# Kernel optimization log

Measured on AMD Instinct MI355X. Metric: run time of the kernel, lower is better.

## Reference

```python
import jax, jax.numpy as jnp
import numpy as np
from jax import lax

FEAT = 384        # features
FFN = 768         # ffn_features (chunk=True -> halves of 384)
ZDIM = FFN // 2   # 384
HID = 192         # AE hidden
B, N = 4, 128
LN_EPS = 1e-5


def gelu(x):
    return jax.nn.gelu(x, approximate=False)  # torch nn.GELU default = exact erf


def setup_inputs() -> dict:
    key = jax.random.key(0)
    ks = jax.random.split(key, 12)

    def lin(k, fan_in, shape):
        bound = 1.0 / np.sqrt(fan_in)
        return jax.random.uniform(k, shape, jnp.float32, -bound, bound)

    return {
        "x": jax.random.normal(ks[0], (B, N, FEAT), jnp.float32),
        "U_w": lin(ks[1], FEAT, (FEAT, FFN)),
        "U_b": lin(ks[2], FEAT, (FFN,)),
        "ln_w": jnp.ones((ZDIM,), jnp.float32),
        "ln_b": jnp.zeros((ZDIM,), jnp.float32),
        "enc_w": lin(ks[3], ZDIM, (ZDIM, HID)),
        "enc_b": lin(ks[4], ZDIM, (HID,)),
        "dec_w": lin(ks[5], HID, (HID, ZDIM)),
        "dec_b": lin(ks[6], HID, (ZDIM,)),
        "V_w": lin(ks[7], ZDIM, (ZDIM, FEAT)),
        "V_b": lin(ks[8], ZDIM, (FEAT,)),
    }


def _ae(z, enc_w, enc_b, dec_w, dec_b):
    h = gelu(z @ enc_w + enc_b)
    return h @ dec_w + dec_b


def reference(x, U_w, U_b, ln_w, ln_b, enc_w, enc_b, dec_w, dec_b, V_w, V_b):
    h = gelu(x @ U_w + U_b)                    # (B,N,FFN)
    xh, z = jnp.split(h, 2, axis=-1)           # chunk=True: (B,N,ZDIM) each
    z = lax.stop_gradient(z)                   # z.detach()
    mu = jnp.mean(z, axis=-1, keepdims=True)
    var = jnp.var(z, axis=-1, keepdims=True)
    z = (z - mu) / jnp.sqrt(var + LN_EPS) * ln_w + ln_b

    n = z.shape[1]
    eye = jnp.eye(n, dtype=z.dtype)
    # z_mask[b,i,j,:] = z[b,j,:] if i==j else 0   (mask_type='zeros')
    z_mask = eye[None, :, :, None] * z[:, None, :, :]   # (B,N,N,ZDIM)
    preds = _ae(z_mask, enc_w, enc_b, dec_w, dec_b)      # (B,N,N,ZDIM)
    dist = jnp.einsum('bijf,bjf->bij', preds, z)         # (B,N,N)
    attn = lax.stop_gradient(jax.nn.softmax(dist, axis=-1))
    out = jnp.einsum('bij,bjf->bif', attn, xh)           # (B,N,ZDIM)
    return out @ V_w + V_b                               # (B,N,FEAT)
```

## Files before the change

kernel.cpp:

```cpp
#include <hip/hip_runtime.h>
#include <hip/hip_bf16.h>
#include <math.h>

#define FEAT 384
#define FFN  768
#define ZDIM 384
#define HID  192
#define BB   4
#define NN   128
#define BN   (BB*NN)

__device__ __forceinline__ float gelu_exact(float x) {
    return 0.5f * x * (1.0f + erff(x * 0.70710678118654752440f));
}

__device__ __forceinline__ float bflo(unsigned u) { return __uint_as_float(u << 16); }
__device__ __forceinline__ float bfhi(unsigned u) { return __uint_as_float(u & 0xFFFF0000u); }

template<bool F32>
__device__ __forceinline__ float ldg(const void* p, int i) {
    if constexpr (F32) return ((const float*)p)[i];
    return __uint_as_float(((unsigned)((const unsigned short*)p)[i]) << 16);
}
template<bool F32>
__device__ __forceinline__ void stg(void* p, size_t i, float v) {
    if constexpr (F32) ((float*)p)[i] = v;
    else ((__hip_bfloat16*)p)[i] = __float2bfloat16(v);
}

template<bool F32> struct V4;
template<> struct V4<true> {
    float4 a;
    __device__ __forceinline__ void load(const void* p, size_t off) {
        a = *(const float4*)((const float*)p + off);
    }
    __device__ __forceinline__ float g(int i) const { return (&a.x)[i]; }
};
template<> struct V4<false> {
    uint2 u;
    __device__ __forceinline__ void load(const void* p, size_t off) {
        u = *(const uint2*)((const unsigned short*)p + off);
    }
    __device__ __forceinline__ float g(int i) const {
        const unsigned w = (&u.x)[i >> 1];
        return (i & 1) ? bfhi(w) : bflo(w);
    }
};

__device__ __forceinline__ bool is_f32(const void* ln_w) {
    return ((const unsigned short*)ln_w)[0] == 0;
}

__device__ __forceinline__ float block_sum(float v, float* sm) {
    for (int o = 32; o > 0; o >>= 1) v += __shfl_down(v, o, 64);
    const int lane = threadIdx.x & 63, w = threadIdx.x >> 6;
    __syncthreads();
    if (lane == 0) sm[w] = v;
    __syncthreads();
    return sm[0] + sm[1] + sm[2] + sm[3] + sm[4] + sm[5];
}
__device__ __forceinline__ float block_max(float v, float* sm) {
    for (int o = 32; o > 0; o >>= 1) v = fmaxf(v, __shfl_down(v, o, 64));
    const int lane = threadIdx.x & 63, w = threadIdx.x >> 6;
    __syncthreads();
    if (lane == 0) sm[w] = v;
    __syncthreads();
    return fmaxf(fmaxf(fmaxf(sm[0], sm[1]), fmaxf(sm[2], sm[3])), fmaxf(sm[4], sm[5]));
}
__device__ __forceinline__ void block_sum8(const float v[8], float* sm, float out[8]) {
    float tv[8];
    #pragma unroll
    for (int n = 0; n < 8; n++) tv[n] = v[n];
    for (int o = 32; o > 0; o >>= 1) {
        #pragma unroll
        for (int n = 0; n < 8; n++) tv[n] += __shfl_down(tv[n], o, 64);
    }
    const int lane = threadIdx.x & 63, w = threadIdx.x >> 6;
    __syncthreads();
    if (lane == 0) {
        #pragma unroll
        for (int n = 0; n < 8; n++) sm[n * 6 + w] = tv[n];
    }
    __syncthreads();
    #pragma unroll
    for (int n = 0; n < 8; n++)
        out[n] = sm[n*6] + sm[n*6+1] + sm[n*6+2] + sm[n*6+3] + sm[n*6+4] + sm[n*6+5];
}

#define SM_TOTAL 9840

template<bool F32, int KCH, int M>
__device__ __forceinline__ void gemmMx4(
    const void* __restrict__ W, int ldw, int c0, int kb,
    const float* __restrict__ in, int ldin, float acc[M][4])
{
    constexpr int NB = KCH / 8;
    V4<F32> buf[3][8];
    #pragma unroll
    for (int j = 0; j < 8; j++) buf[0][j].load(W, (size_t)(kb + j) * ldw + c0);
    if (NB > 1) {
        #pragma unroll
        for (int j = 0; j < 8; j++) buf[1][j].load(W, (size_t)(kb + 8 + j) * ldw + c0);
    }
    #pragma unroll
    for (int b = 0; b < NB; b++) {
        const int cur = b % 3;
        if (b + 2 < NB) {
            const int nxt = (b + 2) % 3;
            #pragma unroll
            for (int j = 0; j < 8; j++)
                buf[nxt][j].load(W, (size_t)(kb + (b + 2) * 8 + j) * ldw + c0);
        }
        #pragma unroll
        for (int m = 0; m < M; m++) {
            const float4 x0 = *(const float4*)(in + m * ldin + kb + b * 8);
            const float4 x1 = *(const float4*)(in + m * ldin + kb + b * 8 + 4);
            const float xv[8] = {x0.x, x0.y, x0.z, x0.w, x1.x, x1.y, x1.z, x1.w};
            #pragma unroll
            for (int j = 0; j < 8; j++) {
                #pragma unroll
                for (int i = 0; i < 4; i++)
                    acc[m][i] = fmaf(xv[j], buf[cur][j].g(i), acc[m][i]);
            }
        }
    }
}

template<bool F32>
__device__ void bodyA(float* S, int q,
    const void* __restrict__ x, const void* __restrict__ U_w,
    const void* __restrict__ U_b, const void* __restrict__ ln_w,
    const void* __restrict__ ln_b, const void* __restrict__ enc_w,
    const void* __restrict__ enc_b, const void* __restrict__ dec_w,
    const void* __restrict__ dec_b,
    float* __restrict__ d0, float* __restrict__ diag)
{
    const int rb = 4 * q;
    const int t = threadIdx.x;
    float* xs = S;
    float* zs = S + 1536;
    float* hid = S + 3072;
    float* gh = S + 3840;
    float* part = S + 4032;
    float* sm = S + 9792;

    #pragma unroll
    for (int m = 0; m < 4; m++) xs[m * 384 + t] = ldg<F32>(x, (rb + m) * FEAT + t);
    if (t < HID) gh[t] = gelu_exact(ldg<F32>(enc_b, t));
    __syncthreads();

    const int cg = t % 96, kh = t / 96;
    const int cL = 4 * cg, cG = ZDIM + cL, kb = 96 * kh;
    float acc[4][4] = {};
    gemmMx4<F32, 96, 4>(U_w, FFN, cG, kb, xs, 384, acc);
    if (kh > 0) {
        float* p = &part[(kh - 1) * 1536 + cg];
        #pragma unroll
        for (int m = 0; m < 4; m++)
            #pragma unroll
            for (int i = 0; i < 4; i++) p[(m * 4 + i) * 96] = acc[m][i];
    }
    __syncthreads();

    float hv[4][4];
    float sv[8] = {};
    if (kh == 0) {
        #pragma unroll
        for (int i = 0; i < 4; i++) {
            const float ub = ldg<F32>(U_b, cG + i);
            #pragma unroll
            for (int m = 0; m < 4; m++) {
                float v = acc[m][i] + ub
                        + part[(m * 4 + i) * 96 + cg]
                        + part[1536 + (m * 4 + i) * 96 + cg]
                        + part[3072 + (m * 4 + i) * 96 + cg];
                v = gelu_exact(v);
                hv[m][i] = v;
                sv[m] += v;
                sv[4 + m] += v * v;
            }
        }
    }
    float SS[8];
    block_sum8(sv, sm, SS);
    if (kh == 0) {
        #pragma unroll
        for (int m = 0; m < 4; m++) {
            const float mu = SS[m] * (1.0f / ZDIM);
            const float rs = rsqrtf(SS[4 + m] * (1.0f / ZDIM) - mu * mu + 1e-5f);
            #pragma unroll
            for (int i = 0; i < 4; i++) {
                const int zc = cL + i;
                zs[m * 384 + zc] = (hv[m][i] - mu) * rs * ldg<F32>(ln_w, zc) + ldg<F32>(ln_b, zc);
            }
        }
    }
    __syncthreads();

    {
        const int cgE = t % 48, khE = t / 48;
        const int cE = 4 * cgE, kbE = 48 * khE;
        float ea[4][4] = {};
        gemmMx4<F32, 48, 4>(enc_w, HID, cE, kbE, zs, 384, ea);
        if (khE > 0) {
            float* p = &part[(khE - 1) * 768 + cgE];
            #pragma unroll
            for (int m = 0; m < 4; m++)
                #pragma unroll
                for (int i = 0; i < 4; i++) p[(m * 4 + i) * 48] = ea[m][i];
        }
        __syncthreads();
        if (khE == 0) {
            #pragma unroll
            for (int i = 0; i < 4; i++) {
                const float ebv = ldg<F32>(enc_b, cE + i);
                #pragma unroll
                for (int m = 0; m < 4; m++) {
                    float v = ea[m][i] + ebv;
                    #pragma unroll
                    for (int kk = 0; kk < 7; kk++)
                        v += part[kk * 768 + (m * 4 + i) * 48 + cgE];
                    hid[m * 192 + cE + i] = gelu_exact(v);
                }
            }
        }
        __syncthreads();
    }

    {
        const int cgD = t % 96, khD = t / 96;
        const int cD = 4 * cgD, kbD = 48 * khD;
        float da[5][4] = {};
        gemmMx4<F32, 48, 5>(dec_w, ZDIM, cD, kbD, hid, 192, da);
        if (khD > 0) {
            float* p = &part[(khD - 1) * 1920 + cgD];
            #pragma unroll
            for (int m = 0; m < 5; m++)
                #pragma unroll
                for (int i = 0; i < 4; i++) p[(m * 4 + i) * 96] = da[m][i];
        }
        __syncthreads();
        float dv[8] = {};
        if (khD == 0) {
            #pragma unroll
            for (int i = 0; i < 4; i++) {
                const int c = cD + i;
                const float dbv = ldg<F32>(dec_b, c);
                float vc = da[4][i] + dbv;
                #pragma unroll
                for (int kk = 0; kk < 3; kk++)
                    vc += part[kk * 1920 + (16 + i) * 96 + cgD];
                #pragma unroll
                for (int m = 0; m < 4; m++) {
                    float v = da[m][i] + dbv;
                    #pragma unroll
                    for (int kk = 0; kk < 3; kk++)
                        v += part[kk * 1920 + (m * 4 + i) * 96 + cgD];
                    const float zv = zs[m * 384 + c];
                    dv[m] = fmaf(v, zv, dv[m]);
                    dv[4 + m] = fmaf(vc, zv, dv[4 + m]);
                }
            }
        }
        float DD8[8];
        block_sum8(dv, sm, DD8);
        if (t == 0) {
            #pragma unroll
            for (int m = 0; m < 4; m++) { diag[rb + m] = DD8[m]; d0[rb + m] = DD8[4 + m]; }
        }
    }
}

template<bool F32>
__device__ void bodyB(float* S, int q,
    const void* __restrict__ x, const void* __restrict__ U_w,
    const void* __restrict__ U_b, const void* __restrict__ V_w,
    float* __restrict__ Y)
{
    const int rb = 4 * q;
    const int t = threadIdx.x;
    float* xs = S;
    float* zs = S + 1536;
    float* part = S + 4032;

    #pragma unroll
    for (int m = 0; m < 4; m++) xs[m * 384 + t] = ldg<F32>(x, (rb + m) * FEAT + t);
    __syncthreads();

    const int cg = t % 96, kh = t / 96;
    const int cL = 4 * cg, kb = 96 * kh;
    float acc[4][4] = {};
    gemmMx4<F32, 96, 4>(U_w, FFN, cL, kb, xs, 384, acc);
    if (kh > 0) {
        float* p = &part[(kh - 1) * 1536 + cg];
        #pragma unroll
        for (int m = 0; m < 4; m++)
            #pragma unroll
            for (int i = 0; i < 4; i++) p[(m * 4 + i) * 96] = acc[m][i];
    }
    __syncthreads();
    if (kh == 0) {
        #pragma unroll
        for (int i = 0; i < 4; i++) {
            const float ub = ldg<F32>(U_b, cL + i);
            #pragma unroll
            for (int m = 0; m < 4; m++) {
                float v = acc[m][i] + ub
                        + part[(m * 4 + i) * 96 + cg]
                        + part[1536 + (m * 4 + i) * 96 + cg]
                        + part[3072 + (m * 4 + i) * 96 + cg];
                zs[m * 384 + cL + i] = gelu_exact(v);
            }
        }
    }
    __syncthreads();

    float ya[4][4] = {};
    gemmMx4<F32, 96, 4>(V_w, FEAT, cL, kb, zs, 384, ya);
    if (kh > 0) {
        float* p = &part[(kh - 1) * 1536 + cg];
        #pragma unroll
        for (int m = 0; m < 4; m++)
            #pragma unroll
            for (int i = 0; i < 4; i++) p[(m * 4 + i) * 96] = ya[m][i];
    }
    __syncthreads();
    if (kh == 0) {
        #pragma unroll
        for (int m = 0; m < 4; m++) {
            float o[4];
            #pragma unroll
            for (int i = 0; i < 4; i++) {
                o[i] = ya[m][i]
                     + part[(m * 4 + i) * 96 + cg]
                     + part[1536 + (m * 4 + i) * 96 + cg]
                     + part[3072 + (m * 4 + i) * 96 + cg];
            }
            *(float4*)(Y + (size_t)(rb + m) * FEAT + cL) = make_float4(o[0], o[1], o[2], o[3]);
        }
    }
}

__global__ __launch_bounds__(384) void k_main(
    const void* x, const void* U_w, const void* U_b,
    const void* ln_w, const void* ln_b,
    const void* enc_w, const void* enc_b,
    const void* dec_w, const void* dec_b, const void* V_w,
    float* Y, float* d0, float* diag)
{
    __shared__ float S[SM_TOTAL];
    const int type = blockIdx.x & 1;
    const int q = blockIdx.x >> 1;
    if (is_f32(ln_w)) {
        if (type == 0) bodyA<true >(S, q, x, U_w, U_b, ln_w, ln_b, enc_w, enc_b, dec_w, dec_b, d0, diag);
        else           bodyB<true >(S, q, x, U_w, U_b, V_w, Y);
    } else {
        if (type == 0) bodyA<false>(S, q, x, U_w, U_b, ln_w, ln_b, enc_w, enc_b, dec_w, dec_b, d0, diag);
        else           bodyB<false>(S, q, x, U_w, U_b, V_w, Y);
    }
}

template<bool F32>
__device__ void combine_body(
    const float* __restrict__ d0, const float* __restrict__ diag,
    const float* __restrict__ Y,
    const void* __restrict__ V_b, void* __restrict__ out)
{
    const int b  = blockIdx.x >> 4;
    const int cc = (blockIdx.x & 15) * 24;
    const int t = threadIdx.x;
    const int c = t % 24, qq = t / 24;
    __shared__ float e0s[NN], eds[NN];
    __shared__ float bp[16 * 24];
    __shared__ float baseY[24];
    __shared__ float sm[12];

    float d0v = -INFINITY, dgv = -INFINITY;
    if (t < NN) { d0v = d0[b * NN + t]; dgv = diag[b * NN + t]; }
    const float m = block_max(fmaxf(d0v, dgv), sm);
    float e0v = 0.f;
    if (t < NN) {
        e0v = expf(d0v - m);
        e0s[t] = e0v;
        eds[t] = expf(dgv - m);
    }
    const float S = block_sum(e0v, sm);

    const float* Yb = Y + (size_t)b * NN * FEAT + cc + c;
    const int j0 = 8 * qq;
    float w[8];
    #pragma unroll
    for (int j = 0; j < 8; j++) w[j] = Yb[(size_t)(j0 + j) * FEAT];
    float p = 0.f;
    #pragma unroll
    for (int j = 0; j < 8; j++) p = fmaf(e0s[j0 + j], w[j], p);
    bp[qq * 24 + c] = p;
    __syncthreads();
    if (qq == 0) {
        float s = 0.f;
        #pragma unroll
        for (int g = 0; g < 16; g++) s += bp[g * 24 + c];
        baseY[c] = s;
    }
    __syncthreads();

    const float bY = baseY[c];
    const float vb = ldg<F32>(V_b, cc + c);
    #pragma unroll
    for (int j = 0; j < 8; j++) {
        const int r = j0 + j;
        const float inv = 1.0f / (S - e0s[r] + eds[r]);
        const float val = (bY + (eds[r] - e0s[r]) * w[j]) * inv + vb;
        stg<F32>(out, (size_t)(b * NN + r) * FEAT + cc + c, val);
    }
}

__global__ __launch_bounds__(384) void k_combine(
    const void* ln_w,
    const float* d0, const float* diag, const float* Y,
    const void* V_b, void* out)
{
    if (is_f32(ln_w))
        combine_body<true >(d0, diag, Y, V_b, out);
    else
        combine_body<false>(d0, diag, Y, V_b, out);
}

extern "C" void kernel_launch(void* const* d_in, const int* in_sizes, int n_in,
                              void* d_out, int out_size, void* d_ws, size_t ws_size,
                              hipStream_t stream) {
    const void* x     = d_in[0];
    const void* U_w   = d_in[1];
    const void* U_b   = d_in[2];
    const void* ln_w  = d_in[3];
    const void* ln_b  = d_in[4];
    const void* enc_w = d_in[5];
    const void* enc_b = d_in[6];
    const void* dec_w = d_in[7];
    const void* dec_b = d_in[8];
    const void* V_w   = d_in[9];
    const void* V_b   = d_in[10];

    float* ws   = (float*)d_ws;
    float* Y    = ws;
    float* d0   = Y + (size_t)BN * FEAT;
    float* diag = d0 + BN;

    k_main<<<2 * (BN / 4), 384, 0, stream>>>(x, U_w, U_b, ln_w, ln_b, enc_w, enc_b,
                                             dec_w, dec_b, V_w, Y, d0, diag);
    k_combine<<<16 * BB, 384, 0, stream>>>(ln_w, d0, diag, Y, V_b, d_out);
}
```

Baseline: 103.3 us.

## Split fused main kernel into two stages with 8-row tiles and algebraic AE dot

Replaces the single fused kernel (256 blocks of 4 rows each) with two kernels. Stage 1 computes U-projection tiles of 8 rows by 96 columns across 512 blocks and transposes enc_w/dec_w into a combined weight buffer. Stage 2 runs the LayerNorm plus autoencoder path and the V-projection as 8-row blocks split over hidden or column tiles, with the AE diagonal term written as gelu(enc)·(dec_w·z) partial sums reduced in the combine kernel. The aim is more parallelism and better weight reuse per block. The cost is an extra launch and global round-trips for xh, z0 and the weight transpose.

```diff
diff --git a/kernel.cpp b/kernel.cpp
--- a/kernel.cpp
+++ b/kernel.cpp
@@ -10,6 +10,7 @@
 #define NN   128
 #define BN   (BB*NN)
 
+
 __device__ __forceinline__ float gelu_exact(float x) {
     return 0.5f * x * (1.0f + erff(x * 0.70710678118654752440f));
 }
@@ -18,7 +19,7 @@
 __device__ __forceinline__ float bfhi(unsigned u) { return __uint_as_float(u & 0xFFFF0000u); }
 
 template<bool F32>
-__device__ __forceinline__ float ldg(const void* p, int i) {
+__device__ __forceinline__ float ldg(const void* p, size_t i) {
     if constexpr (F32) return ((const float*)p)[i];
     return __uint_as_float(((unsigned)((const unsigned short*)p)[i]) << 16);
 }
@@ -47,6 +48,19 @@
     }
 };
 
+template<bool F32>
+__device__ __forceinline__ void load8(const void* p, size_t i, float o[8]) {
+    if constexpr (F32) {
+        const float4 a = *(const float4*)((const float*)p + i);
+        const float4 b = *(const float4*)((const float*)p + i + 4);
+        o[0]=a.x;o[1]=a.y;o[2]=a.z;o[3]=a.w;o[4]=b.x;o[5]=b.y;o[6]=b.z;o[7]=b.w;
+    } else {
+        const uint4 u = *(const uint4*)((const unsigned short*)p + i);
+        o[0]=bflo(u.x);o[1]=bfhi(u.x);o[2]=bflo(u.y);o[3]=bfhi(u.y);
+        o[4]=bflo(u.z);o[5]=bfhi(u.z);o[6]=bflo(u.w);o[7]=bfhi(u.w);
+    }
+}
+
 __device__ __forceinline__ bool is_f32(const void* ln_w) {
     return ((const unsigned short*)ln_w)[0] == 0;
 }
@@ -67,55 +81,52 @@
     __syncthreads();
     return fmaxf(fmaxf(fmaxf(sm[0], sm[1]), fmaxf(sm[2], sm[3])), fmaxf(sm[4], sm[5]));
 }
-__device__ __forceinline__ void block_sum8(const float v[8], float* sm, float out[8]) {
-    float tv[8];
-    #pragma unroll
-    for (int n = 0; n < 8; n++) tv[n] = v[n];
+__device__ __forceinline__ void block_sum16(const float v[16], float* sm, float out[16]) {
+    float tv[16];
+    #pragma unroll
+    for (int n = 0; n < 16; n++) tv[n] = v[n];
     for (int o = 32; o > 0; o >>= 1) {
         #pragma unroll
-        for (int n = 0; n < 8; n++) tv[n] += __shfl_down(tv[n], o, 64);
+        for (int n = 0; n < 16; n++) tv[n] += __shfl_down(tv[n], o, 64);
     }
     const int lane = threadIdx.x & 63, w = threadIdx.x >> 6;
     __syncthreads();
     if (lane == 0) {
         #pragma unroll
-        for (int n = 0; n < 8; n++) sm[n * 6 + w] = tv[n];
-    }
-    __syncthreads();
-    #pragma unroll
-    for (int n = 0; n < 8; n++)
+        for (int n = 0; n < 16; n++) sm[n * 6 + w] = tv[n];
+    }
+    __syncthreads();
+    #pragma unroll
+    for (int n = 0; n < 16; n++)
         out[n] = sm[n*6] + sm[n*6+1] + sm[n*6+2] + sm[n*6+3] + sm[n*6+4] + sm[n*6+5];
 }
 
-#define SM_TOTAL 9840
-
-template<bool F32, int KCH, int M>
-__device__ __forceinline__ void gemmMx4(
-    const void* __restrict__ W, int ldw, int c0, int kb,
-    const float* __restrict__ in, int ldin, float acc[M][4])
-{
-    constexpr int NB = KCH / 8;
-    V4<F32> buf[3][8];
-    #pragma unroll
-    for (int j = 0; j < 8; j++) buf[0][j].load(W, (size_t)(kb + j) * ldw + c0);
-    if (NB > 1) {
-        #pragma unroll
-        for (int j = 0; j < 8; j++) buf[1][j].load(W, (size_t)(kb + 8 + j) * ldw + c0);
-    }
-    #pragma unroll
-    for (int b = 0; b < NB; b++) {
-        const int cur = b % 3;
-        if (b + 2 < NB) {
-            const int nxt = (b + 2) % 3;
+template<bool F32>
+__device__ __forceinline__ void tile_gemm_8x96(
+    const void* __restrict__ W, int ldw, int c0,
+    const float* __restrict__ xs, float* __restrict__ part, float out2[2])
+{
+    const int t = threadIdx.x;
+    const int cg = t % 24, kh = t / 24;
+    const int kb = kh * 24;
+    const int cc = c0 + 4 * cg;
+    float acc[8][4] = {};
+    V4<F32> buf[2][8];
+    #pragma unroll
+    for (int j = 0; j < 8; j++) buf[0][j].load(W, (size_t)(kb + j) * ldw + cc);
+    #pragma unroll
+    for (int b = 0; b < 3; b++) {
+        const int cur = b & 1;
+        if (b < 2) {
             #pragma unroll
             for (int j = 0; j < 8; j++)
-                buf[nxt][j].load(W, (size_t)(kb + (b + 2) * 8 + j) * ldw + c0);
-        }
-        #pragma unroll
-        for (int m = 0; m < M; m++) {
-            const float4 x0 = *(const float4*)(in + m * ldin + kb + b * 8);
-            const float4 x1 = *(const float4*)(in + m * ldin + kb + b * 8 + 4);
-            const float xv[8] = {x0.x, x0.y, x0.z, x0.w, x1.x, x1.y, x1.z, x1.w};
+                buf[cur ^ 1][j].load(W, (size_t)(kb + 8 * (b + 1) + j) * ldw + cc);
+        }
+        #pragma unroll
+        for (int m = 0; m < 8; m++) {
+            const float4 x0 = *(const float4*)(xs + m * 384 + kb + 8 * b);
+            const float4 x1 = *(const float4*)(xs + m * 384 + kb + 8 * b + 4);
+            const float xv[8] = {x0.x,x0.y,x0.z,x0.w,x1.x,x1.y,x1.z,x1.w};
             #pragma unroll
             for (int j = 0; j < 8; j++) {
                 #pragma unroll
@@ -124,245 +135,226 @@
             }
         }
     }
-}
-
-template<bool F32>
-__device__ void bodyA(float* S, int q,
-    const void* __restrict__ x, const void* __restrict__ U_w,
-    const void* __restrict__ U_b, const void* __restrict__ ln_w,
-    const void* __restrict__ ln_b, const void* __restrict__ enc_w,
-    const void* __restrict__ enc_b, const void* __restrict__ dec_w,
-    const void* __restrict__ dec_b,
-    float* __restrict__ d0, float* __restrict__ diag)
-{
-    const int rb = 4 * q;
+    #pragma unroll
+    for (int m = 0; m < 8; m++)
+        *(float4*)(part + kh * 768 + m * 96 + 4 * cg) =
+            make_float4(acc[m][0], acc[m][1], acc[m][2], acc[m][3]);
+    __syncthreads();
+    #pragma unroll
+    for (int s = 0; s < 2; s++) {
+        const int u = t + 384 * s;
+        float v = 0.f;
+        #pragma unroll
+        for (int k2 = 0; k2 < 16; k2++) v += part[k2 * 768 + u];
+        out2[s] = v;
+    }
+}
+
+#define S_LDS 15360
+
+template<bool F32>
+__device__ void stage1_body(const void* __restrict__ x, const void* __restrict__ U_w,
+                            const void* __restrict__ U_b,
+                            const void* __restrict__ enc_w, const void* __restrict__ dec_w,
+                            float* __restrict__ xh, float* __restrict__ z0,
+                            float* __restrict__ WEG, float* S)
+{
+    const int bid = blockIdx.x, t = threadIdx.x;
+    if (bid >= 512) {
+        if (bid < 560) {
+            const int h0 = (bid - 512) * 4;
+            V4<F32> w; w.load(enc_w, (size_t)t * HID + h0);
+            #pragma unroll
+            for (int j = 0; j < 4; j++) WEG[(size_t)(h0 + j) * 384 + t] = w.g(j);
+        } else {
+            const int r0 = (bid - 560) * 4;
+            #pragma unroll
+            for (int j = 0; j < 4; j++)
+                WEG[(size_t)(192 + r0 + j) * 384 + t] =
+                    ldg<F32>(dec_w, (size_t)(r0 + j) * ZDIM + t);
+        }
+        return;
+    }
+    float* xs = S;
+    float* part = S + 3072;
+    const int rowg = bid >> 3, colt = bid & 7;
+    const int rb = rowg * 8;
+    {
+        const int r = t / 48, c8 = 8 * (t % 48);
+        float xv[8]; load8<F32>(x, (size_t)(rb + r) * FEAT + c8, xv);
+        #pragma unroll
+        for (int j = 0; j < 8; j++) xs[r * 384 + c8 + j] = xv[j];
+    }
+    __syncthreads();
+    float out2[2];
+    tile_gemm_8x96<F32>(U_w, FFN, colt * 96, xs, part, out2);
+    const int uhalf = (colt >= 4);
+    float* dst = uhalf ? z0 : xh;
+    const int cbase = colt * 96 - (uhalf ? 384 : 0);
+    #pragma unroll
+    for (int s = 0; s < 2; s++) {
+        const int u = t + 384 * s;
+        const int m = u / 96, col = u % 96;
+        const float v = out2[s] + ldg<F32>(U_b, colt * 96 + col);
+        dst[(size_t)(rb + m) * 384 + cbase + col] = gelu_exact(v);
+    }
+}
+
+template<bool F32>
+__device__ void stage2z_body(const void* __restrict__ ln_w, const void* __restrict__ ln_b,
+                             const void* __restrict__ enc_b, const void* __restrict__ dec_b,
+                             const float* __restrict__ z0, const float* __restrict__ WEG,
+                             float* __restrict__ d0p, float* __restrict__ dgp,
+                             float* S, int q)
+{
+    const int rowg = q >> 2, ht = q & 3;
+    const int rb = rowg * 8, h0 = ht * 48;
+    const int t = threadIdx.x;
+    float* zs  = S;
+    float* pEG = S + 3072;
+    float* Es  = S + 6144;
+    float* Gs  = S + 6528;
+    float* sm  = S + 6912;
+
+    const int r = t / 48, c8 = 8 * (t % 48);
+    float zv[8];
+    {
+        const float4 a = *(const float4*)(z0 + (size_t)(rb + r) * 384 + c8);
+        const float4 b = *(const float4*)(z0 + (size_t)(rb + r) * 384 + c8 + 4);
+        zv[0]=a.x;zv[1]=a.y;zv[2]=a.z;zv[3]=a.w;zv[4]=b.x;zv[5]=b.y;zv[6]=b.z;zv[7]=b.w;
+    }
+    float s1 = 0.f, s2 = 0.f;
+    #pragma unroll
+    for (int j = 0; j < 8; j++) { s1 += zv[j]; s2 += zv[j] * zv[j]; }
+    float sv[16] = {}; sv[r] = s1; sv[8 + r] = s2;
+    float SS[16];
+    block_sum16(sv, sm, SS);
+    const float mu = SS[r] * (1.0f / ZDIM);
+    const float rs = rsqrtf(SS[8 + r] * (1.0f / ZDIM) - mu * mu + 1e-5f);
+    float lw[8], lb[8];
+    load8<F32>(ln_w, c8, lw);
+    load8<F32>(ln_b, c8, lb);
+    #pragma unroll
+    for (int j = 0; j < 8; j++)
+        zs[r * 384 + c8 + j] = (zv[j] - mu) * rs * lw[j] + lb[j];
+    __syncthreads();
+
+    const int hg = t % 96, kh = t / 96;
+    const int wrow = h0 + hg + (hg < 48 ? 0 : 144);
+    const float* Wr = WEG + (size_t)wrow * 384 + kh * 96;
+    float acc[8] = {};
+    float4 wb[2][4];
+    #pragma unroll
+    for (int j = 0; j < 4; j++) wb[0][j] = *(const float4*)(Wr + 4 * j);
+    #pragma unroll
+    for (int g = 0; g < 6; g++) {
+        const int cur = g & 1;
+        if (g < 5) {
+            #pragma unroll
+            for (int j = 0; j < 4; j++)
+                wb[cur ^ 1][j] = *(const float4*)(Wr + 16 * (g + 1) + 4 * j);
+        }
+        #pragma unroll
+        for (int j = 0; j < 4; j++) {
+            const int k = kh * 96 + 16 * g + 4 * j;
+            const float4 wq = wb[cur][j];
+            #pragma unroll
+            for (int rr = 0; rr < 8; rr++) {
+                const float4 zq = *(const float4*)(zs + rr * 384 + k);
+                acc[rr] = fmaf(zq.x, wq.x, fmaf(zq.y, wq.y,
+                          fmaf(zq.z, wq.z, fmaf(zq.w, wq.w, acc[rr]))));
+            }
+        }
+    }
+    #pragma unroll
+    for (int rr = 0; rr < 8; rr++) pEG[kh * 768 + rr * 96 + hg] = acc[rr];
+    __syncthreads();
+    #pragma unroll
+    for (int s = 0; s < 2; s++) {
+        const int u = t + 384 * s;
+        const int ur = u / 96, uh = u % 96;
+        const float v = pEG[u] + pEG[768 + u] + pEG[1536 + u] + pEG[2304 + u];
+        if (uh < 48) Es[ur * 48 + uh] = v + ldg<F32>(enc_b, h0 + uh);
+        else         Gs[ur * 48 + uh - 48] = v;
+    }
+    __syncthreads();
+    const int pr = t / 48, ph = t % 48;
+    const float gv = Gs[pr * 48 + ph];
+    float pd = gelu_exact(Es[pr * 48 + ph]) * gv;
+    float p0 = gelu_exact(ldg<F32>(enc_b, h0 + ph)) * gv;
+    if (ht == 0) {
+        float dbz = 0.f;
+        #pragma unroll
+        for (int j = 0; j < 8; j++) {
+            const int c = ph + 48 * j;
+            dbz = fmaf(ldg<F32>(dec_b, c), zs[pr * 384 + c], dbz);
+        }
+        pd += dbz; p0 += dbz;
+    }
+    float sv2[16] = {}; sv2[pr] = pd; sv2[8 + pr] = p0;
+    float SS2[16];
+    block_sum16(sv2, sm, SS2);
+    if (t < 8)            dgp[ht * BN + rb + t] = SS2[t];
+    else if (t < 16)      d0p[ht * BN + rb + (t - 8)] = SS2[8 + (t - 8)];
+}
+
+template<bool F32>
+__device__ void stage2y_body(const void* __restrict__ V_w, const float* __restrict__ xh,
+                             float* __restrict__ Y, float* S, int q)
+{
+    const int rowg = q >> 2, colt = q & 3;
+    const int rb = rowg * 8, c0 = colt * 96;
     const int t = threadIdx.x;
     float* xs = S;
-    float* zs = S + 1536;
-    float* hid = S + 3072;
-    float* gh = S + 3840;
-    float* part = S + 4032;
-    float* sm = S + 9792;
-
-    #pragma unroll
-    for (int m = 0; m < 4; m++) xs[m * 384 + t] = ldg<F32>(x, (rb + m) * FEAT + t);
-    if (t < HID) gh[t] = gelu_exact(ldg<F32>(enc_b, t));
-    __syncthreads();
-
-    const int cg = t % 96, kh = t / 96;
-    const int cL = 4 * cg, cG = ZDIM + cL, kb = 96 * kh;
-    float acc[4][4] = {};
-    gemmMx4<F32, 96, 4>(U_w, FFN, cG, kb, xs, 384, acc);
-    if (kh > 0) {
-        float* p = &part[(kh - 1) * 1536 + cg];
-        #pragma unroll
-        for (int m = 0; m < 4; m++)
-            #pragma unroll
-            for (int i = 0; i < 4; i++) p[(m * 4 + i) * 96] = acc[m][i];
-    }
-    __syncthreads();
-
-    float hv[4][4];
-    float sv[8] = {};
-    if (kh == 0) {
-        #pragma unroll
-        for (int i = 0; i < 4; i++) {
-            const float ub = ldg<F32>(U_b, cG + i);
-            #pragma unroll
-            for (int m = 0; m < 4; m++) {
-                float v = acc[m][i] + ub
-                        + part[(m * 4 + i) * 96 + cg]
-                        + part[1536 + (m * 4 + i) * 96 + cg]
-                        + part[3072 + (m * 4 + i) * 96 + cg];
-                v = gelu_exact(v);
-                hv[m][i] = v;
-                sv[m] += v;
-                sv[4 + m] += v * v;
-            }
-        }
-    }
-    float SS[8];
-    block_sum8(sv, sm, SS);
-    if (kh == 0) {
-        #pragma unroll
-        for (int m = 0; m < 4; m++) {
-            const float mu = SS[m] * (1.0f / ZDIM);
-            const float rs = rsqrtf(SS[4 + m] * (1.0f / ZDIM) - mu * mu + 1e-5f);
-            #pragma unroll
-            for (int i = 0; i < 4; i++) {
-                const int zc = cL + i;
-                zs[m * 384 + zc] = (hv[m][i] - mu) * rs * ldg<F32>(ln_w, zc) + ldg<F32>(ln_b, zc);
-            }
-        }
-    }
-    __syncthreads();
-
+    float* part = S + 3072;
     {
-        const int cgE = t % 48, khE = t / 48;
-        const int cE = 4 * cgE, kbE = 48 * khE;
-        float ea[4][4] = {};
-        gemmMx4<F32, 48, 4>(enc_w, HID, cE, kbE, zs, 384, ea);
-        if (khE > 0) {
-            float* p = &part[(khE - 1) * 768 + cgE];
-            #pragma unroll
-            for (int m = 0; m < 4; m++)
-                #pragma unroll
-                for (int i = 0; i < 4; i++) p[(m * 4 + i) * 48] = ea[m][i];
-        }
-        __syncthreads();
-        if (khE == 0) {
-            #pragma unroll
-            for (int i = 0; i < 4; i++) {
-                const float ebv = ldg<F32>(enc_b, cE + i);
-                #pragma unroll
-                for (int m = 0; m < 4; m++) {
-                    float v = ea[m][i] + ebv;
-                    #pragma unroll
-                    for (int kk = 0; kk < 7; kk++)
-                        v += part[kk * 768 + (m * 4 + i) * 48 + cgE];
-                    hid[m * 192 + cE + i] = gelu_exact(v);
-                }
-            }
-        }
-        __syncthreads();
-    }
-
-    {
-        const int cgD = t % 96, khD = t / 96;
-        const int cD = 4 * cgD, kbD = 48 * khD;
-        float da[5][4] = {};
-        gemmMx4<F32, 48, 5>(dec_w, ZDIM, cD, kbD, hid, 192, da);
-        if (khD > 0) {
-            float* p = &part[(khD - 1) * 1920 + cgD];
-            #pragma unroll
-            for (int m = 0; m < 5; m++)
-                #pragma unroll
-                for (int i = 0; i < 4; i++) p[(m * 4 + i) * 96] = da[m][i];
-        }
-        __syncthreads();
-        float dv[8] = {};
-        if (khD == 0) {
-            #pragma unroll
-            for (int i = 0; i < 4; i++) {
-                const int c = cD + i;
-                const float dbv = ldg<F32>(dec_b, c);
-                float vc = da[4][i] + dbv;
-                #pragma unroll
-                for (int kk = 0; kk < 3; kk++)
-                    vc += part[kk * 1920 + (16 + i) * 96 + cgD];
-                #pragma unroll
-                for (int m = 0; m < 4; m++) {
-                    float v = da[m][i] + dbv;
-                    #pragma unroll
-                    for (int kk = 0; kk < 3; kk++)
-                        v += part[kk * 1920 + (m * 4 + i) * 96 + cgD];
-                    const float zv = zs[m * 384 + c];
-                    dv[m] = fmaf(v, zv, dv[m]);
-                    dv[4 + m] = fmaf(vc, zv, dv[4 + m]);
-                }
-            }
-        }
-        float DD8[8];
-        block_sum8(dv, sm, DD8);
-        if (t == 0) {
-            #pragma unroll
-            for (int m = 0; m < 4; m++) { diag[rb + m] = DD8[m]; d0[rb + m] = DD8[4 + m]; }
-        }
-    }
-}
-
-template<bool F32>
-__device__ void bodyB(float* S, int q,
-    const void* __restrict__ x, const void* __restrict__ U_w,
-    const void* __restrict__ U_b, const void* __restrict__ V_w,
-    float* __restrict__ Y)
-{
-    const int rb = 4 * q;
-    const int t = threadIdx.x;
-    float* xs = S;
-    float* zs = S + 1536;
-    float* part = S + 4032;
-
-    #pragma unroll
-    for (int m = 0; m < 4; m++) xs[m * 384 + t] = ldg<F32>(x, (rb + m) * FEAT + t);
-    __syncthreads();
-
-    const int cg = t % 96, kh = t / 96;
-    const int cL = 4 * cg, kb = 96 * kh;
-    float acc[4][4] = {};
-    gemmMx4<F32, 96, 4>(U_w, FFN, cL, kb, xs, 384, acc);
-    if (kh > 0) {
-        float* p = &part[(kh - 1) * 1536 + cg];
-        #pragma unroll
-        for (int m = 0; m < 4; m++)
-            #pragma unroll
-            for (int i = 0; i < 4; i++) p[(m * 4 + i) * 96] = acc[m][i];
-    }
-    __syncthreads();
-    if (kh == 0) {
-        #pragma unroll
-        for (int i = 0; i < 4; i++) {
-            const float ub = ldg<F32>(U_b, cL + i);
-            #pragma unroll
-            for (int m = 0; m < 4; m++) {
-                float v = acc[m][i] + ub
-                        + part[(m * 4 + i) * 96 + cg]
-                        + part[1536 + (m * 4 + i) * 96 + cg]
-                        + part[3072 + (m * 4 + i) * 96 + cg];
-                zs[m * 384 + cL + i] = gelu_exact(v);
-            }
-        }
-    }
-    __syncthreads();
-
-    float ya[4][4] = {};
-    gemmMx4<F32, 96, 4>(V_w, FEAT, cL, kb, zs, 384, ya);
-    if (kh > 0) {
-        float* p = &part[(kh - 1) * 1536 + cg];
-        #pragma unroll
-        for (int m = 0; m < 4; m++)
-            #pragma unroll
-            for (int i = 0; i < 4; i++) p[(m * 4 + i) * 96] = ya[m][i];
-    }
-    __syncthreads();
-    if (kh == 0) {
-        #pragma unroll
-        for (int m = 0; m < 4; m++) {
-            float o[4];
-            #pragma unroll
-            for (int i = 0; i < 4; i++) {
-                o[i] = ya[m][i]
-                     + part[(m * 4 + i) * 96 + cg]
-                     + part[1536 + (m * 4 + i) * 96 + cg]
-                     + part[3072 + (m * 4 + i) * 96 + cg];
-            }
-            *(float4*)(Y + (size_t)(rb + m) * FEAT + cL) = make_float4(o[0], o[1], o[2], o[3]);
-        }
-    }
-}
-
-__global__ __launch_bounds__(384) void k_main(
-    const void* x, const void* U_w, const void* U_b,
-    const void* ln_w, const void* ln_b,
-    const void* enc_w, const void* enc_b,
-    const void* dec_w, const void* dec_b, const void* V_w,
-    float* Y, float* d0, float* diag)
-{
-    __shared__ float S[SM_TOTAL];
-    const int type = blockIdx.x & 1;
-    const int q = blockIdx.x >> 1;
+        const int r = t / 48, c8 = 8 * (t % 48);
+        const float4 a = *(const float4*)(xh + (size_t)(rb + r) * 384 + c8);
+        const float4 b = *(const float4*)(xh + (size_t)(rb + r) * 384 + c8 + 4);
+        *(float4*)(xs + r * 384 + c8) = a;
+        *(float4*)(xs + r * 384 + c8 + 4) = b;
+    }
+    __syncthreads();
+    float out2[2];
+    tile_gemm_8x96<F32>(V_w, FEAT, c0, xs, part, out2);
+    #pragma unroll
+    for (int s = 0; s < 2; s++) {
+        const int u = t + 384 * s;
+        const int m = u / 96, col = u % 96;
+        Y[(size_t)(rb + m) * 384 + c0 + col] = out2[s];
+    }
+}
+
+__global__ __launch_bounds__(384, 3) void k_stage1(
+    const void* x, const void* U_w, const void* U_b, const void* ln_w,
+    const void* enc_w, const void* dec_w,
+    float* xh, float* z0, float* WEG)
+{
+    __shared__ float S[S_LDS];
+    if (is_f32(ln_w)) stage1_body<true >(x, U_w, U_b, enc_w, dec_w, xh, z0, WEG, S);
+    else              stage1_body<false>(x, U_w, U_b, enc_w, dec_w, xh, z0, WEG, S);
+}
+
+__global__ __launch_bounds__(384, 3) void k_stage2(
+    const void* ln_w, const void* ln_b, const void* enc_b, const void* dec_b,
+    const void* V_w, const float* xh, const float* z0, const float* WEG,
+    float* Y, float* d0p, float* dgp)
+{
+    __shared__ float S[S_LDS];
+    const int type = blockIdx.x >> 8;
+    const int q = blockIdx.x & 255;
     if (is_f32(ln_w)) {
-        if (type == 0) bodyA<true >(S, q, x, U_w, U_b, ln_w, ln_b, enc_w, enc_b, dec_w, dec_b, d0, diag);
-        else           bodyB<true >(S, q, x, U_w, U_b, V_w, Y);
+        if (type == 0) stage2z_body<true >(ln_w, ln_b, enc_b, dec_b, z0, WEG, d0p, dgp, S, q);
+        else           stage2y_body<true >(V_w, xh, Y, S, q);
     } else {
-        if (type == 0) bodyA<false>(S, q, x, U_w, U_b, ln_w, ln_b, enc_w, enc_b, dec_w, dec_b, d0, diag);
-        else           bodyB<false>(S, q, x, U_w, U_b, V_w, Y);
+        if (type == 0) stage2z_body<false>(ln_w, ln_b, enc_b, dec_b, z0, WEG, d0p, dgp, S, q);
+        else           stage2y_body<false>(V_w, xh, Y, S, q);
     }
 }
 
 template<bool F32>
 __device__ void combine_body(
-    const float* __restrict__ d0, const float* __restrict__ diag,
+    const float* __restrict__ d0p, const float* __restrict__ dgp,
     const float* __restrict__ Y,
     const void* __restrict__ V_b, void* __restrict__ out)
 {
@@ -376,7 +368,15 @@
     __shared__ float sm[12];
 
     float d0v = -INFINITY, dgv = -INFINITY;
-    if (t < NN) { d0v = d0[b * NN + t]; dgv = diag[b * NN + t]; }
+    if (t < NN) {
+        float a0 = 0.f, ag = 0.f;
+        #pragma unroll
+        for (int ct = 0; ct < 4; ct++) {
+            a0 += d0p[ct * BN + b * NN + t];
+            ag += dgp[ct * BN + b * NN + t];
+        }
+        d0v = a0; dgv = ag;
+    }
     const float m = block_max(fmaxf(d0v, dgv), sm);
     float e0v = 0.f;
     if (t < NN) {
@@ -384,7 +384,7 @@
         e0s[t] = e0v;
         eds[t] = expf(dgv - m);
     }
-    const float S = block_sum(e0v, sm);
+    const float Ssum = block_sum(e0v, sm);
 
     const float* Yb = Y + (size_t)b * NN * FEAT + cc + c;
     const int j0 = 8 * qq;
@@ -409,7 +409,7 @@
     #pragma unroll
     for (int j = 0; j < 8; j++) {
         const int r = j0 + j;
-        const float inv = 1.0f / (S - e0s[r] + eds[r]);
+        const float inv = 1.0f / (Ssum - e0s[r] + eds[r]);
         const float val = (bY + (eds[r] - e0s[r]) * w[j]) * inv + vb;
         stg<F32>(out, (size_t)(b * NN + r) * FEAT + cc + c, val);
     }
@@ -417,13 +417,13 @@
 
 __global__ __launch_bounds__(384) void k_combine(
     const void* ln_w,
-    const float* d0, const float* diag, const float* Y,
+    const float* d0p, const float* dgp, const float* Y,
     const void* V_b, void* out)
 {
     if (is_f32(ln_w))
-        combine_body<true >(d0, diag, Y, V_b, out);
+        combine_body<true >(d0p, dgp, Y, V_b, out);
     else
-        combine_body<false>(d0, diag, Y, V_b, out);
+        combine_body<false>(d0p, dgp, Y, V_b, out);
 }
 
 extern "C" void kernel_launch(void* const* d_in, const int* in_sizes, int n_in,
@@ -441,12 +441,15 @@
     const void* V_w   = d_in[9];
     const void* V_b   = d_in[10];
 
-    float* ws   = (float*)d_ws;
-    float* Y    = ws;
-    float* d0   = Y + (size_t)BN * FEAT;
-    float* diag = d0 + BN;
-
-    k_main<<<2 * (BN / 4), 384, 0, stream>>>(x, U_w, U_b, ln_w, ln_b, enc_w, enc_b,
-                                             dec_w, dec_b, V_w, Y, d0, diag);
-    k_combine<<<16 * BB, 384, 0, stream>>>(ln_w, d0, diag, Y, V_b, d_out);
-}
+    float* ws  = (float*)d_ws;
+    float* xh  = ws;
+    float* z0  = xh  + 196608;
+    float* WEG = z0  + 196608;
+    float* Y   = WEG + 147456;
+    float* d0p = Y   + 196608;
+    float* dgp = d0p + 4 * BN;
+
+    k_stage1<<<608, 384, 0, stream>>>(x, U_w, U_b, ln_w, enc_w, dec_w, xh, z0, WEG);
+    k_stage2<<<512, 384, 0, stream>>>(ln_w, ln_b, enc_b, dec_b, V_w, xh, z0, WEG, Y, d0p, dgp);
+    k_combine<<<16 * BB, 384, 0, stream>>>(ln_w, d0p, dgp, Y, V_b, d_out);
+}
```

New measurement: 111.6 us. 1.08x slower.

## Fuse combine stage into main kernel via cooperative grid sync

Applied to the files above, without the earlier changes.

Merges the separate combine kernel into the main kernel. A cooperative launch and a grid-wide barrier replace the second kernel launch, and the first 64 blocks run the softmax/combine step after the barrier. This removes one launch and the gap between kernels. In exchange, all 256 blocks must be co-resident, and a grid sync on this hardware carries its own cost, which may match or exceed the launch gap it replaces.

```diff
diff --git a/kernel.cpp b/kernel.cpp
--- a/kernel.cpp
+++ b/kernel.cpp
@@ -1,5 +1,6 @@
 #include <hip/hip_runtime.h>
 #include <hip/hip_bf16.h>
+#include <hip/hip_cooperative_groups.h>
 #include <math.h>
 
 #define FEAT 384
@@ -341,27 +342,8 @@
     }
 }
 
-__global__ __launch_bounds__(384) void k_main(
-    const void* x, const void* U_w, const void* U_b,
-    const void* ln_w, const void* ln_b,
-    const void* enc_w, const void* enc_b,
-    const void* dec_w, const void* dec_b, const void* V_w,
-    float* Y, float* d0, float* diag)
-{
-    __shared__ float S[SM_TOTAL];
-    const int type = blockIdx.x & 1;
-    const int q = blockIdx.x >> 1;
-    if (is_f32(ln_w)) {
-        if (type == 0) bodyA<true >(S, q, x, U_w, U_b, ln_w, ln_b, enc_w, enc_b, dec_w, dec_b, d0, diag);
-        else           bodyB<true >(S, q, x, U_w, U_b, V_w, Y);
-    } else {
-        if (type == 0) bodyA<false>(S, q, x, U_w, U_b, ln_w, ln_b, enc_w, enc_b, dec_w, dec_b, d0, diag);
-        else           bodyB<false>(S, q, x, U_w, U_b, V_w, Y);
-    }
-}
-
 template<bool F32>
-__device__ void combine_body(
+__device__ void combine_body(float* S,
     const float* __restrict__ d0, const float* __restrict__ diag,
     const float* __restrict__ Y,
     const void* __restrict__ V_b, void* __restrict__ out)
@@ -370,10 +352,11 @@
     const int cc = (blockIdx.x & 15) * 24;
     const int t = threadIdx.x;
     const int c = t % 24, qq = t / 24;
-    __shared__ float e0s[NN], eds[NN];
-    __shared__ float bp[16 * 24];
-    __shared__ float baseY[24];
-    __shared__ float sm[12];
+    float* e0s   = S;
+    float* eds   = S + 128;
+    float* bp    = S + 256;
+    float* baseY = S + 640;
+    float* sm    = S + 664;
 
     float d0v = -INFINITY, dgv = -INFINITY;
     if (t < NN) { d0v = d0[b * NN + t]; dgv = diag[b * NN + t]; }
@@ -384,7 +367,7 @@
         e0s[t] = e0v;
         eds[t] = expf(dgv - m);
     }
-    const float S = block_sum(e0v, sm);
+    const float Ssum = block_sum(e0v, sm);
 
     const float* Yb = Y + (size_t)b * NN * FEAT + cc + c;
     const int j0 = 8 * qq;
@@ -409,21 +392,39 @@
     #pragma unroll
     for (int j = 0; j < 8; j++) {
         const int r = j0 + j;
-        const float inv = 1.0f / (S - e0s[r] + eds[r]);
+        const float inv = 1.0f / (Ssum - e0s[r] + eds[r]);
         const float val = (bY + (eds[r] - e0s[r]) * w[j]) * inv + vb;
         stg<F32>(out, (size_t)(b * NN + r) * FEAT + cc + c, val);
     }
 }
 
-__global__ __launch_bounds__(384) void k_combine(
-    const void* ln_w,
-    const float* d0, const float* diag, const float* Y,
-    const void* V_b, void* out)
+__global__ __launch_bounds__(384) void k_main(
+    const void* x, const void* U_w, const void* U_b,
+    const void* ln_w, const void* ln_b,
+    const void* enc_w, const void* enc_b,
+    const void* dec_w, const void* dec_b, const void* V_w,
+    const void* V_b,
+    float* Y, float* d0, float* diag, void* out)
 {
-    if (is_f32(ln_w))
-        combine_body<true >(d0, diag, Y, V_b, out);
-    else
-        combine_body<false>(d0, diag, Y, V_b, out);
+    __shared__ float S[SM_TOTAL];
+    const bool f32 = is_f32(ln_w);
+    const int type = blockIdx.x & 1;
+    const int q = blockIdx.x >> 1;
+    if (f32) {
+        if (type == 0) bodyA<true >(S, q, x, U_w, U_b, ln_w, ln_b, enc_w, enc_b, dec_w, dec_b, d0, diag);
+        else           bodyB<true >(S, q, x, U_w, U_b, V_w, Y);
+    } else {
+        if (type == 0) bodyA<false>(S, q, x, U_w, U_b, ln_w, ln_b, enc_w, enc_b, dec_w, dec_b, d0, diag);
+        else           bodyB<false>(S, q, x, U_w, U_b, V_w, Y);
+    }
+
+    __threadfence();
+    cooperative_groups::this_grid().sync();
+
+    if (blockIdx.x < 64) {
+        if (f32) combine_body<true >(S, d0, diag, Y, V_b, out);
+        else     combine_body<false>(S, d0, diag, Y, V_b, out);
+    }
 }
 
 extern "C" void kernel_launch(void* const* d_in, const int* in_sizes, int n_in,
@@ -445,8 +446,14 @@
     float* Y    = ws;
     float* d0   = Y + (size_t)BN * FEAT;
     float* diag = d0 + BN;
-
-    k_main<<<2 * (BN / 4), 384, 0, stream>>>(x, U_w, U_b, ln_w, ln_b, enc_w, enc_b,
-                                             dec_w, dec_b, V_w, Y, d0, diag);
-    k_combine<<<16 * BB, 384, 0, stream>>>(ln_w, d0, diag, Y, V_b, d_out);
-}
+    void*  out  = d_out;
+
+    void* args[] = {
+        (void*)&x, (void*)&U_w, (void*)&U_b, (void*)&ln_w, (void*)&ln_b,
+        (void*)&enc_w, (void*)&enc_b, (void*)&dec_w, (void*)&dec_b,
+        (void*)&V_w, (void*)&V_b,
+        (void*)&Y, (void*)&d0, (void*)&diag, (void*)&out
+    };
+    hipLaunchCooperativeKernel((const void*)k_main, dim3(2 * (BN / 4)), dim3(384),
+                               args, 0, stream);
+}
```

Measured after the change: 180.6 us. 74.8% more time.
